# Performance work log

Hardware: AMD Instinct MI355X
Metric: run time of the kernel (lower is better)

Reference implementation:

```python
import jax, jax.numpy as jnp
import numpy as np

WS = 8          # window_size
NH = 8          # num_heads
DIM = 512
EPS = 1e-5


def _layernorm(x, gamma, beta):
    mu = jnp.mean(x, axis=-1, keepdims=True)
    var = jnp.mean(jnp.square(x - mu), axis=-1, keepdims=True)
    return (x - mu) * jax.lax.rsqrt(var + EPS) * gamma + beta


def setup_inputs() -> dict:
    key = jax.random.key(0)
    ks = jax.random.split(key, 16)
    B, C, H, W = 8, DIM, 128, 128
    s = 0.02
    return {
        "x": jax.random.normal(ks[0], (B, C, H, W), jnp.float32),
        "gamma1": jnp.ones((C,), jnp.float32),
        "beta1": jnp.zeros((C,), jnp.float32),
        "gamma2": jnp.ones((C,), jnp.float32),
        "beta2": jnp.zeros((C,), jnp.float32),
        "w_qkv": jax.random.normal(ks[1], (C, 3 * C), jnp.float32) * s,
        "b_qkv": jnp.zeros((3 * C,), jnp.float32),
        "w_out": jax.random.normal(ks[2], (C, C), jnp.float32) * s,
        "b_out": jnp.zeros((C,), jnp.float32),
        "w1": jax.random.normal(ks[3], (C, 4 * C), jnp.float32) * s,
        "b1": jnp.zeros((4 * C,), jnp.float32),
        "w2": jax.random.normal(ks[4], (4 * C, C), jnp.float32) * s,
        "b2": jnp.zeros((C,), jnp.float32),
    }


def reference(x, gamma1, beta1, gamma2, beta2, w_qkv, b_qkv, w_out, b_out, w1, b1, w2, b2):
    B, C, H, W = x.shape
    hd = C // NH          # head_dim = 64
    L = WS * WS           # tokens per window = 64
    N = (H // WS) * (W // WS)

    # window_partition: (B,C,H,W) -> (B,N,C,ws,ws)
    xw = x.reshape(B, C, H // WS, WS, W // WS, WS)
    xw = xw.transpose(0, 1, 2, 4, 3, 5).reshape(B, C, N, WS, WS).transpose(0, 2, 1, 3, 4)
    # spatial_flatten -> (B,N,L,C)
    t = xw.reshape(B, N, C, L).transpose(0, 1, 3, 2)

    # --- attention (non-transposed path) ---
    xn = _layernorm(t, gamma1, beta1)
    qkv = jnp.einsum('bnlc,cd->bnld', xn, w_qkv) + b_qkv
    qkv = qkv.reshape(B, N, L, 3, NH, hd).transpose(3, 0, 1, 4, 2, 5)  # (3,B,N,H,L,hd)
    q, k, v = qkv[0], qkv[1], qkv[2]
    # note: module scales by 1/head_dim on BOTH q and k -> 1/hd^2 total
    scores = jnp.einsum('bnhld,bnhmd->bnhlm', q, k) / (hd * hd)
    attn = jax.nn.softmax(scores, axis=-1)
    o = jnp.einsum('bnhlm,bnhmd->bnhld', attn, v)
    o = o.transpose(0, 1, 3, 2, 4).reshape(B, N, L, C)
    o = jnp.einsum('bnlc,cd->bnld', o, w_out) + b_out
    t = t + o

    # --- MLP ---
    xn2 = _layernorm(t, gamma2, beta2)
    h = jax.nn.gelu(jnp.einsum('bnlc,cd->bnld', xn2, w1) + b1, approximate=False)
    t = t + jnp.einsum('bnld,dc->bnlc', h, w2) + b2

    # spatial_unflatten + window_unpartition -> (B,C,H,W)
    y = t.transpose(0, 1, 3, 2).reshape(B, N, C, WS, WS).transpose(0, 2, 1, 3, 4)
    y = y.reshape(B, C, H // WS, W // WS, WS, WS).transpose(0, 1, 2, 4, 3, 5).reshape(B, C, H, W)
    return y
```

## Files before the change

### kernel.cpp

```cpp
#include <hip/hip_runtime.h>
#include <cstdint>
#include <cstddef>


typedef unsigned short u16;
typedef unsigned int u32;
typedef __attribute__((ext_vector_type(4))) float f32x4;
typedef __attribute__((ext_vector_type(8))) short bf16x8;

#define DEVINL __device__ __forceinline__

DEVINL float bf2f(u16 u){ union { u32 i; float f; } v; v.i = ((u32)u) << 16; return v.f; }
DEVINL u16 f2bf(float f){
  union { float f; u32 i; } v; v.f = f;
  u32 u = v.i;
  u32 r = (u + 0x7fffu + ((u >> 16) & 1u)) >> 16;
  return (u16)r;
}

DEVINL void gload16(u16* lds, const void* g){
  __builtin_amdgcn_global_load_lds(
      (__attribute__((address_space(1))) u32*)(g),
      (__attribute__((address_space(3))) u32*)(lds), 16, 0, 0);
}

__global__ __launch_bounds__(256) void wt_kernel(const float* __restrict__ in,
                                                 u16* __restrict__ out, int K, int N)
{
  __shared__ float tile[64][65];
  int tiles_n = N >> 6;
  int tk = blockIdx.x / tiles_n, tn = blockIdx.x % tiles_n;
  int k0 = tk * 64, n0 = tn * 64;
  int lane = threadIdx.x & 63, wr = threadIdx.x >> 6;
#pragma unroll
  for (int i = 0; i < 16; i++){
    int r = wr * 16 + i;
    tile[r][lane] = in[(size_t)(k0 + r) * N + n0 + lane];
  }
  __syncthreads();
#pragma unroll
  for (int i = 0; i < 16; i++){
    int r = wr * 16 + i;
    out[(size_t)(n0 + r) * K + k0 + lane] = f2bf(tile[lane][r]);
  }
}

template<int MODE>
__global__ __launch_bounds__(256) void ln_kernel(
    const float* __restrict__ x, const u16* __restrict__ o2,
    const float* __restrict__ gamma, const float* __restrict__ beta,
    u16* __restrict__ out)
{
  __shared__ u16 sm[512 * 64];
  int wg = blockIdx.x;
  int b = wg >> 8, n = wg & 255, wy = n >> 4, wx = n & 15;
  int t = threadIdx.x, l = t & 63, wv = t >> 6;
  int yy = l >> 3, xx = l & 7;
  size_t xbase = ((size_t)b * 512) * 16384 + (size_t)(wy * 8 + yy) * 128 + wx * 8 + xx;

#pragma unroll 4
  for (int i = 0; i < 128; i++){
    int c = wv * 128 + i;
    float v = x[xbase + (size_t)c * 16384];
    sm[c * 64 + (l ^ ((2 * (c >> 3)) & 63))] = f2bf(v);
  }
  __syncthreads();

  size_t gbase = (size_t)wg * 64;
  int lane = l;
  int c0 = lane * 8;
  int fs = (2 * lane) & 63;
  float g8[8], b8[8];
#pragma unroll
  for (int j = 0; j < 8; j++){ g8[j] = gamma[c0 + j]; b8[j] = beta[c0 + j]; }

  for (int it = 0; it < 16; it++){
    int tok = wv * 16 + it;
    int lidx = tok ^ fs;
    u16 oarr[8];
    if (MODE == 1){
      uint4 ov = *(const uint4*)&o2[(gbase + tok) * 512 + c0];
      *(uint4*)oarr = ov;
    }
    float tv[8]; float sum = 0.f, sq = 0.f;
#pragma unroll
    for (int j = 0; j < 8; j++){
      float v = bf2f(sm[(c0 + j) * 64 + lidx]);
      if (MODE == 1) v += bf2f(oarr[j]);
      tv[j] = v; sum += v; sq += v * v;
    }
#pragma unroll
    for (int d = 1; d < 64; d <<= 1){
      sum += __shfl_xor(sum, d, 64);
      sq  += __shfl_xor(sq, d, 64);
    }
    float mu = sum * (1.0f / 512.0f);
    float var = sq * (1.0f / 512.0f) - mu * mu;
    float rs = rsqrtf(var + 1e-5f);
    u16 r8[8];
#pragma unroll
    for (int j = 0; j < 8; j++) r8[j] = f2bf((tv[j] - mu) * rs * g8[j] + b8[j]);
    *(uint4*)&out[(gbase + tok) * 512 + c0] = *(uint4*)r8;
  }
}

template<int EPI>
__global__ __launch_bounds__(256) void gemm_kernel(
    const u16* __restrict__ A, const u16* __restrict__ BT,
    const float* __restrict__ bias, const u16* __restrict__ ADD,
    u16* __restrict__ Cout, int M, int N, int K)
{
  (void)M;
  __shared__ u16 As[128 * 32];
  __shared__ u16 Bs[128 * 32];
  const int nbn = N >> 7;
  int bm = blockIdx.x / nbn, bn = blockIdx.x % nbn;
  size_t m0 = (size_t)bm * 128; int n0 = bn * 128;
  int lane = threadIdx.x & 63, wv = threadIdx.x >> 6;
  int wr = wv >> 1, wc = wv & 1;

  f32x4 zero4 = {0.f, 0.f, 0.f, 0.f};
  f32x4 acc[4][4];
#pragma unroll
  for (int i = 0; i < 4; i++)
#pragma unroll
    for (int j = 0; j < 4; j++) acc[i][j] = zero4;

  int srow = wv * 16 + (lane >> 2);
  int skc = (lane & 3) * 8;
  const u16* Abase = A + m0 * K + skc;
  const u16* Bbase = BT + (size_t)n0 * K + skc;

  for (int kt = 0; kt < K; kt += 32){
    gload16(&As[wv * 512],        Abase + (size_t)srow * K + kt);
    gload16(&As[2048 + wv * 512], Abase + (size_t)(srow + 64) * K + kt);
    gload16(&Bs[wv * 512],        Bbase + (size_t)srow * K + kt);
    gload16(&Bs[2048 + wv * 512], Bbase + (size_t)(srow + 64) * K + kt);
    __syncthreads();

    bf16x8 af[4], bfr[4];
    int rb = (lane & 15) * 32 + (lane >> 4) * 8;
#pragma unroll
    for (int mt = 0; mt < 4; mt++) af[mt]  = *(const bf16x8*)&As[(wr * 64 + mt * 16) * 32 + rb];
#pragma unroll
    for (int nt = 0; nt < 4; nt++) bfr[nt] = *(const bf16x8*)&Bs[(wc * 64 + nt * 16) * 32 + rb];
#pragma unroll
    for (int mt = 0; mt < 4; mt++)
#pragma unroll
      for (int nt = 0; nt < 4; nt++)
        acc[mt][nt] = __builtin_amdgcn_mfma_f32_16x16x32_bf16(af[mt], bfr[nt], acc[mt][nt], 0, 0, 0);
    __syncthreads();
  }

#pragma unroll
  for (int nt = 0; nt < 4; nt++){
    int c = n0 + wc * 64 + nt * 16 + (lane & 15);
    float bv = bias[c];
#pragma unroll
    for (int mt = 0; mt < 4; mt++){
      size_t r0 = m0 + wr * 64 + mt * 16 + ((lane >> 4) * 4);
#pragma unroll
      for (int reg = 0; reg < 4; reg++){
        float v = acc[mt][nt][reg] + bv;
        if (EPI == 1) v = 0.5f * v * (1.0f + erff(v * 0.70710678118654752f));
        size_t idx = (r0 + reg) * (size_t)N + c;
        if (EPI == 2) v += bf2f(ADD[idx]);
        Cout[idx] = f2bf(v);
      }
    }
  }
}

__global__ __launch_bounds__(64) void attn_kernel(const u16* __restrict__ QKV,
                                                  u16* __restrict__ O)
{
  __shared__ u16 qs[4096], ks2[4096], vs[4096], ps[4096];
  int blk = blockIdx.x;
  int wg = blk >> 3, h = blk & 7;
  size_t g0 = (size_t)wg * 64;
  int lane = threadIdx.x;
  int lr = lane >> 3, lch = lane & 7;

#pragma unroll
  for (int it = 0; it < 8; it++){
    int r = it * 8 + lr;
    int sc = lch ^ (r & 7);
    {
      uint4 d = *(const uint4*)&QKV[(g0 + r) * 1536 + h * 64 + lch * 8];
      *(uint4*)&qs[r * 64 + sc * 8] = d;
    }
    {
      uint4 d = *(const uint4*)&QKV[(g0 + r) * 1536 + 512 + h * 64 + lch * 8];
      *(uint4*)&ks2[r * 64 + sc * 8] = d;
    }
    {
      uint4 d = *(const uint4*)&QKV[(g0 + r) * 1536 + 1024 + h * 64 + lch * 8];
      u16 e[8]; *(uint4*)e = d;
      int m = r;
#pragma unroll
      for (int j = 0; j < 8; j++){
        int dd = lch * 8 + j;
        int off = dd * 64 + ((((m * 2) ^ ((dd & 7) << 4))) >> 1);
        vs[off] = e[j];
      }
    }
  }
  __syncthreads();

  f32x4 zero4 = {0.f, 0.f, 0.f, 0.f};
  f32x4 s[4][4];
#pragma unroll
  for (int i = 0; i < 4; i++)
#pragma unroll
    for (int j = 0; j < 4; j++) s[i][j] = zero4;

#pragma unroll
  for (int ks = 0; ks < 2; ks++){
    bf16x8 aq[4], bk[4];
#pragma unroll
    for (int mt = 0; mt < 4; mt++){
      int r = mt * 16 + (lane & 15);
      int cb = (ks * 64 + (lane >> 4) * 16) ^ ((r & 7) << 4);
      aq[mt] = *(const bf16x8*)&qs[r * 64 + (cb >> 1)];
    }
#pragma unroll
    for (int nt = 0; nt < 4; nt++){
      int r = nt * 16 + (lane & 15);
      int cb = (ks * 64 + (lane >> 4) * 16) ^ ((r & 7) << 4);
      bk[nt] = *(const bf16x8*)&ks2[r * 64 + (cb >> 1)];
    }
#pragma unroll
    for (int mt = 0; mt < 4; mt++)
#pragma unroll
      for (int nt = 0; nt < 4; nt++)
        s[mt][nt] = __builtin_amdgcn_mfma_f32_16x16x32_bf16(aq[mt], bk[nt], s[mt][nt], 0, 0, 0);
  }

  const float scl = 1.0f / 4096.0f;
#pragma unroll
  for (int mt = 0; mt < 4; mt++){
#pragma unroll
    for (int reg = 0; reg < 4; reg++){
      float mx = -1e30f;
#pragma unroll
      for (int nt = 0; nt < 4; nt++){
        float v = s[mt][nt][reg] * scl; s[mt][nt][reg] = v; mx = fmaxf(mx, v);
      }
#pragma unroll
      for (int d = 1; d < 16; d <<= 1) mx = fmaxf(mx, __shfl_xor(mx, d, 64));
      float sum = 0.f;
#pragma unroll
      for (int nt = 0; nt < 4; nt++){
        float e = __expf(s[mt][nt][reg] - mx); s[mt][nt][reg] = e; sum += e;
      }
#pragma unroll
      for (int d = 1; d < 16; d <<= 1) sum += __shfl_xor(sum, d, 64);
      float inv = 1.0f / sum;
#pragma unroll
      for (int nt = 0; nt < 4; nt++) s[mt][nt][reg] *= inv;
    }
  }

#pragma unroll
  for (int mt = 0; mt < 4; mt++)
#pragma unroll
    for (int reg = 0; reg < 4; reg++){
      int r = mt * 16 + ((lane >> 4) * 4) + reg;
#pragma unroll
      for (int nt = 0; nt < 4; nt++){
        int c = nt * 16 + (lane & 15);
        ps[r * 64 + ((((c * 2) ^ ((r & 7) << 4))) >> 1)] = f2bf(s[mt][nt][reg]);
      }
    }
  __syncthreads();

  f32x4 o[4][4];
#pragma unroll
  for (int i = 0; i < 4; i++)
#pragma unroll
    for (int j = 0; j < 4; j++) o[i][j] = zero4;

#pragma unroll
  for (int ks = 0; ks < 2; ks++){
    bf16x8 ap[4], bv[4];
#pragma unroll
    for (int mt = 0; mt < 4; mt++){
      int r = mt * 16 + (lane & 15);
      int cb = (ks * 64 + (lane >> 4) * 16) ^ ((r & 7) << 4);
      ap[mt] = *(const bf16x8*)&ps[r * 64 + (cb >> 1)];
    }
#pragma unroll
    for (int nt = 0; nt < 4; nt++){
      int dd = nt * 16 + (lane & 15);
      int cb = (ks * 64 + (lane >> 4) * 16) ^ ((dd & 7) << 4);
      bv[nt] = *(const bf16x8*)&vs[dd * 64 + (cb >> 1)];
    }
#pragma unroll
    for (int mt = 0; mt < 4; mt++)
#pragma unroll
      for (int nt = 0; nt < 4; nt++)
        o[mt][nt] = __builtin_amdgcn_mfma_f32_16x16x32_bf16(ap[mt], bv[nt], o[mt][nt], 0, 0, 0);
  }

#pragma unroll
  for (int mt = 0; mt < 4; mt++)
#pragma unroll
    for (int reg = 0; reg < 4; reg++){
      size_t l = mt * 16 + ((lane >> 4) * 4) + reg;
#pragma unroll
      for (int nt = 0; nt < 4; nt++){
        int dd = nt * 16 + (lane & 15);
        O[(g0 + l) * 512 + h * 64 + dd] = f2bf(o[mt][nt][reg]);
      }
    }
}

__global__ __launch_bounds__(256) void scatter_kernel(
    const float* __restrict__ x, const u16* __restrict__ ms, float* __restrict__ y)
{
  __shared__ u16 sm[512 * 64];
  int wg = blockIdx.x;
  int b = wg >> 8, n = wg & 255, wy = n >> 4, wx = n & 15;
  int t = threadIdx.x, lane = t & 63, wv = t >> 6;
  size_t gbase = (size_t)wg * 64;
  int c0 = lane * 8, fs = (2 * lane) & 63;

  for (int it = 0; it < 16; it++){
    int tok = wv * 16 + it;
    uint4 d = *(const uint4*)&ms[(gbase + tok) * 512 + c0];
    u16 e[8]; *(uint4*)e = d;
    int lidx = tok ^ fs;
#pragma unroll
    for (int j = 0; j < 8; j++) sm[(c0 + j) * 64 + lidx] = e[j];
  }
  __syncthreads();

  int l = lane; int yy = l >> 3, xx = l & 7;
  size_t xbase = ((size_t)b * 512) * 16384 + (size_t)(wy * 8 + yy) * 128 + wx * 8 + xx;
#pragma unroll 4
  for (int i = 0; i < 128; i++){
    int c = wv * 128 + i;
    size_t a = xbase + (size_t)c * 16384;
    y[a] = x[a] + bf2f(sm[c * 64 + (l ^ ((2 * (c >> 3)) & 63))]);
  }
}

extern "C" void kernel_launch(void* const* d_in, const int* in_sizes, int n_in,
                              void* d_out, int out_size, void* d_ws, size_t ws_size,
                              hipStream_t stream)
{
  (void)in_sizes; (void)n_in; (void)out_size; (void)ws_size;
  const float* x      = (const float*)d_in[0];
  const float* gamma1 = (const float*)d_in[1];
  const float* beta1  = (const float*)d_in[2];
  const float* gamma2 = (const float*)d_in[3];
  const float* beta2  = (const float*)d_in[4];
  const float* w_qkv  = (const float*)d_in[5];
  const float* b_qkv  = (const float*)d_in[6];
  const float* w_out  = (const float*)d_in[7];
  const float* b_out  = (const float*)d_in[8];
  const float* w1     = (const float*)d_in[9];
  const float* b1     = (const float*)d_in[10];
  const float* w2     = (const float*)d_in[11];
  const float* b2     = (const float*)d_in[12];
  float* y = (float*)d_out;

  char* ws = (char*)d_ws;
  u16* WqkvT = (u16*)(ws + 0);
  u16* WoutT = (u16*)(ws + 1572864);
  u16* W1T   = (u16*)(ws + 2097152);
  u16* W2T   = (u16*)(ws + 4194304);
  u16* XN    = (u16*)(ws + 6291456);
  u16* O2    = (u16*)(ws + 140509184);
  u16* Obuf  = (u16*)(ws + 274726912);
  u16* QKV   = (u16*)(ws + 408944640);
  u16* Hbuf  = QKV;
  u16* MS    = Obuf;
  const int M = 131072;

  wt_kernel<<<8 * 24, 256, 0, stream>>>(w_qkv, WqkvT, 512, 1536);
  wt_kernel<<<8 * 8,  256, 0, stream>>>(w_out, WoutT, 512, 512);
  wt_kernel<<<8 * 32, 256, 0, stream>>>(w1, W1T, 512, 2048);
  wt_kernel<<<32 * 8, 256, 0, stream>>>(w2, W2T, 2048, 512);

  ln_kernel<0><<<2048, 256, 0, stream>>>(x, nullptr, gamma1, beta1, XN);
  gemm_kernel<0><<<(M / 128) * (1536 / 128), 256, 0, stream>>>(XN, WqkvT, b_qkv, nullptr, QKV, M, 1536, 512);
  attn_kernel<<<16384, 64, 0, stream>>>(QKV, Obuf);
  gemm_kernel<0><<<(M / 128) * (512 / 128), 256, 0, stream>>>(Obuf, WoutT, b_out, nullptr, O2, M, 512, 512);
  ln_kernel<1><<<2048, 256, 0, stream>>>(x, O2, gamma2, beta2, XN);
  gemm_kernel<1><<<(M / 128) * (2048 / 128), 256, 0, stream>>>(XN, W1T, b1, nullptr, Hbuf, M, 2048, 512);
  gemm_kernel<2><<<(M / 128) * (512 / 128), 256, 0, stream>>>(Hbuf, W2T, b2, O2, MS, M, 512, 2048);
  scatter_kernel<<<2048, 256, 0, stream>>>(x, MS, y);
}
```

Before: 2.889 ms.

## Double-buffer GEMM LDS tiles with swizzle, XCD remap, and LDS-staged epilogue

Double-buffers the GEMM's shared-memory tiles so the next K-step's global-to-LDS loads overlap the current MFMAs, removing one barrier per step. It XOR-swizzles the LDS layout to cut bank conflicts and remaps block IDs across the 8 XCDs for cache locality. The epilogue writes results to LDS first and then issues coalesced 16-byte stores, including the residual add. It also replaces the exact erf GELU with a tanh-form sigmoid approximation, which changes numerics slightly.

```diff
diff --git a/kernel.cpp b/kernel.cpp
--- a/kernel.cpp
+++ b/kernel.cpp
@@ -108,13 +108,14 @@
 __global__ __launch_bounds__(256) void gemm_kernel(
     const u16* __restrict__ A, const u16* __restrict__ BT,
     const float* __restrict__ bias, const u16* __restrict__ ADD,
-    u16* __restrict__ Cout, int M, int N, int K)
-{
-  (void)M;
-  __shared__ u16 As[128 * 32];
-  __shared__ u16 Bs[128 * 32];
+    u16* __restrict__ Cout, int N, int K)
+{
+  __shared__ u16 smem[16384];
   const int nbn = N >> 7;
-  int bm = blockIdx.x / nbn, bn = blockIdx.x % nbn;
+  int nwg = gridDim.x;
+  int bid = blockIdx.x;
+  int wgid = (bid & 7) * (nwg >> 3) + (bid >> 3);
+  int bm = wgid / nbn, bn = wgid % nbn;
   size_t m0 = (size_t)bm * 128; int n0 = bn * 128;
   int lane = threadIdx.x & 63, wv = threadIdx.x >> 6;
   int wr = wv >> 1, wc = wv & 1;
@@ -127,46 +128,91 @@
     for (int j = 0; j < 4; j++) acc[i][j] = zero4;
 
   int srow = wv * 16 + (lane >> 2);
-  int skc = (lane & 3) * 8;
-  const u16* Abase = A + m0 * K + skc;
-  const u16* Bbase = BT + (size_t)n0 * K + skc;
-
-  for (int kt = 0; kt < K; kt += 32){
-    gload16(&As[wv * 512],        Abase + (size_t)srow * K + kt);
-    gload16(&As[2048 + wv * 512], Abase + (size_t)(srow + 64) * K + kt);
-    gload16(&Bs[wv * 512],        Bbase + (size_t)srow * K + kt);
-    gload16(&Bs[2048 + wv * 512], Bbase + (size_t)(srow + 64) * K + kt);
-    __syncthreads();
-
+  int scol = (((lane & 3) ^ ((srow >> 1) & 3)) * 8);
+  const u16* Abase = A + m0 * (size_t)K;
+  const u16* Bbase = BT + (size_t)n0 * K;
+
+  auto STAGE = [&](int buf, int kt){
+    u16* as = &smem[buf * 8192];
+    u16* bs = as + 4096;
+    gload16(as + wv * 512,        Abase + (size_t)srow * K + kt + scol);
+    gload16(as + 2048 + wv * 512, Abase + (size_t)(srow + 64) * K + kt + scol);
+    gload16(bs + wv * 512,        Bbase + (size_t)srow * K + kt + scol);
+    gload16(bs + 2048 + wv * 512, Bbase + (size_t)(srow + 64) * K + kt + scol);
+  };
+
+  STAGE(0, 0);
+  __syncthreads();
+
+  int nsteps = K >> 5;
+  int cur = 0;
+  int kslot = lane >> 4;
+  for (int t = 0; t < nsteps; ++t){
+    if (t + 1 < nsteps) STAGE(cur ^ 1, (t + 1) << 5);
+    const u16* as = &smem[cur * 8192];
+    const u16* bs = as + 4096;
     bf16x8 af[4], bfr[4];
-    int rb = (lane & 15) * 32 + (lane >> 4) * 8;
-#pragma unroll
-    for (int mt = 0; mt < 4; mt++) af[mt]  = *(const bf16x8*)&As[(wr * 64 + mt * 16) * 32 + rb];
-#pragma unroll
-    for (int nt = 0; nt < 4; nt++) bfr[nt] = *(const bf16x8*)&Bs[(wc * 64 + nt * 16) * 32 + rb];
+#pragma unroll
+    for (int mt = 0; mt < 4; mt++){
+      int row = wr * 64 + mt * 16 + (lane & 15);
+      af[mt] = *(const bf16x8*)&as[row * 32 + ((kslot ^ ((row >> 1) & 3)) * 8)];
+    }
+#pragma unroll
+    for (int nt = 0; nt < 4; nt++){
+      int row = wc * 64 + nt * 16 + (lane & 15);
+      bfr[nt] = *(const bf16x8*)&bs[row * 32 + ((kslot ^ ((row >> 1) & 3)) * 8)];
+    }
 #pragma unroll
     for (int mt = 0; mt < 4; mt++)
 #pragma unroll
       for (int nt = 0; nt < 4; nt++)
         acc[mt][nt] = __builtin_amdgcn_mfma_f32_16x16x32_bf16(af[mt], bfr[nt], acc[mt][nt], 0, 0, 0);
     __syncthreads();
+    cur ^= 1;
   }
 
 #pragma unroll
   for (int nt = 0; nt < 4; nt++){
-    int c = n0 + wc * 64 + nt * 16 + (lane & 15);
-    float bv = bias[c];
+    int cc = wc * 64 + nt * 16 + (lane & 15);
+    float bv = bias[n0 + cc];
 #pragma unroll
     for (int mt = 0; mt < 4; mt++){
-      size_t r0 = m0 + wr * 64 + mt * 16 + ((lane >> 4) * 4);
+      int r0 = wr * 64 + mt * 16 + ((lane >> 4) * 4);
 #pragma unroll
       for (int reg = 0; reg < 4; reg++){
+        int rr = r0 + reg;
         float v = acc[mt][nt][reg] + bv;
-        if (EPI == 1) v = 0.5f * v * (1.0f + erff(v * 0.70710678118654752f));
-        size_t idx = (r0 + reg) * (size_t)N + c;
-        if (EPI == 2) v += bf2f(ADD[idx]);
-        Cout[idx] = f2bf(v);
-      }
+        if (EPI == 1){
+          float h2 = v * v;
+          float z = -1.5957691216057308f * (v + 0.044715f * v * h2);
+          float e = __expf(z);
+          v = v * __builtin_amdgcn_rcpf(1.0f + e);
+        }
+        smem[rr * 128 + (cc ^ ((rr & 7) << 3))] = f2bf(v);
+      }
+    }
+  }
+  __syncthreads();
+
+  int tr = threadIdx.x >> 2;
+  int tc = threadIdx.x & 3;
+#pragma unroll
+  for (int i = 0; i < 2; i++){
+    int r = i * 64 + tr;
+    size_t gro = (m0 + r) * (size_t)N + n0;
+#pragma unroll
+    for (int j = 0; j < 4; j++){
+      int cw = tc * 8 + j * 32;
+      uint4 d = *(const uint4*)&smem[r * 128 + (cw ^ ((r & 7) << 3))];
+      if (EPI == 2){
+        uint4 av = *(const uint4*)&ADD[gro + cw];
+        u16 de[8], ae[8];
+        *(uint4*)de = d; *(uint4*)ae = av;
+#pragma unroll
+        for (int k = 0; k < 8; k++) de[k] = f2bf(bf2f(de[k]) + bf2f(ae[k]));
+        d = *(uint4*)de;
+      }
+      *(uint4*)&Cout[gro + cw] = d;
     }
   }
 }
@@ -384,11 +430,11 @@
   wt_kernel<<<32 * 8, 256, 0, stream>>>(w2, W2T, 2048, 512);
 
   ln_kernel<0><<<2048, 256, 0, stream>>>(x, nullptr, gamma1, beta1, XN);
-  gemm_kernel<0><<<(M / 128) * (1536 / 128), 256, 0, stream>>>(XN, WqkvT, b_qkv, nullptr, QKV, M, 1536, 512);
+  gemm_kernel<0><<<(M / 128) * (1536 / 128), 256, 0, stream>>>(XN, WqkvT, b_qkv, nullptr, QKV, 1536, 512);
   attn_kernel<<<16384, 64, 0, stream>>>(QKV, Obuf);
-  gemm_kernel<0><<<(M / 128) * (512 / 128), 256, 0, stream>>>(Obuf, WoutT, b_out, nullptr, O2, M, 512, 512);
+  gemm_kernel<0><<<(M / 128) * (512 / 128), 256, 0, stream>>>(Obuf, WoutT, b_out, nullptr, O2, 512, 512);
   ln_kernel<1><<<2048, 256, 0, stream>>>(x, O2, gamma2, beta2, XN);
-  gemm_kernel<1><<<(M / 128) * (2048 / 128), 256, 0, stream>>>(XN, W1T, b1, nullptr, Hbuf, M, 2048, 512);
-  gemm_kernel<2><<<(M / 128) * (512 / 128), 256, 0, stream>>>(Hbuf, W2T, b2, O2, MS, M, 512, 2048);
+  gemm_kernel<1><<<(M / 128) * (2048 / 128), 256, 0, stream>>>(XN, W1T, b1, nullptr, Hbuf, 2048, 512);
+  gemm_kernel<2><<<(M / 128) * (512 / 128), 256, 0, stream>>>(Hbuf, W2T, b2, O2, MS, 512, 2048);
   scatter_kernel<<<2048, 256, 0, stream>>>(x, MS, y);
 }
```

New measurement: 2.457 ms. -14.9%, faster.
